# Kernel tuning notes

Measured on AMD Instinct MI355X. Metric: run time of the kernel, lower is better.

## Reference

```python
import jax, jax.numpy as jnp
import numpy as np

M, T, NX, U = 256, 512, 256, 256


def setup_inputs() -> dict:
    key = jax.random.key(0)
    ks = jax.random.split(key, 8)
    u = lambda k, s: jax.random.uniform(k, s, dtype=jnp.float32) * 0.01
    return {
        "x": jax.random.normal(ks[0], (M, T, NX), dtype=jnp.float32),
        "a0": jax.random.normal(ks[1], (M, U), dtype=jnp.float32),
        "wcx": u(ks[2], (NX, U)),
        "wcc": u(ks[3], (U, U)),
        "bc": jnp.zeros((1, U), jnp.float32),
        "wux": u(ks[4], (NX, U)),
        "wuc": u(ks[5], (U, U)),
        "bu": jnp.zeros((1, U), jnp.float32),
        "wrx": u(ks[6], (NX, U)),
        "wrc": u(ks[7], (U, U)),
        "br": jnp.zeros((1, U), jnp.float32),
    }


def reference(x, a0, wcx, wcc, bc, wux, wuc, bu, wrx, wrc, br):
    # x: [m, t, nx] -> scan over time; state c: [m, units]
    def step(c, xt):
        g_u = jax.nn.sigmoid(c @ wuc + xt @ wux + bu)
        g_r = jax.nn.sigmoid(c @ wrc + xt @ wrx + br)
        # NB: original is (g_r * c_prev) @ wcc due to operator precedence
        cand = jnp.tanh((g_r * c) @ wcc + xt @ wcx + bc)
        c_new = g_u * cand + (1.0 - g_u) * c
        return c_new, None

    c_final, _ = jax.lax.scan(step, a0, jnp.swapaxes(x, 0, 1))
    # return_sequences=False, return_state=False -> last hidden state [m, units]
    return c_final
```

## Files before the change

kernel.cpp:

```cpp
#include <hip/hip_runtime.h>

typedef _Float16 h2 __attribute__((ext_vector_type(2)));
typedef _Float16 h4 __attribute__((ext_vector_type(4)));
typedef _Float16 h8 __attribute__((ext_vector_type(8)));
typedef float f4v __attribute__((ext_vector_type(4)));

#define U_DIM 256
#define M_DIM 256
#define T_DIM 512

#if defined(__has_builtin)
#if __has_builtin(__builtin_amdgcn_fdot2)
#define HAVE_FDOT2 1
#endif
#endif

__device__ __forceinline__ float fdot2f(h2 a, h2 b, float c) {
#ifdef HAVE_FDOT2
  return __builtin_amdgcn_fdot2(a, b, c, false);
#else
  return fmaf((float)a[0], (float)b[0], fmaf((float)a[1], (float)b[1], c));
#endif
}

__device__ __forceinline__ float fast_sigmoid(float z) {
  return __builtin_amdgcn_rcpf(1.f + __expf(-z));
}
__device__ __forceinline__ float fast_tanh(float z) {
  return fmaf(2.f, __builtin_amdgcn_rcpf(1.f + __expf(-2.f * z)), -1.f);
}

__global__ void conv_x(const float* __restrict__ x, h8* __restrict__ x16, int n8) {
  int i = blockIdx.x * 256 + threadIdx.x;
  if (i >= n8) return;
  const float4* p = (const float4*)(x + (size_t)i * 8);
  float4 v0 = p[0], v1 = p[1];
  h8 o = {(_Float16)v0.x, (_Float16)v0.y, (_Float16)v0.z, (_Float16)v0.w,
          (_Float16)v1.x, (_Float16)v1.y, (_Float16)v1.z, (_Float16)v1.w};
  x16[i] = o;
}

__global__ void prep_xw(const float* __restrict__ wux, const float* __restrict__ wrx,
                        const float* __restrict__ wcx, h8* __restrict__ wt16) {
  int idx = blockIdx.x * 256 + threadIdx.x;
  int mtx = idx >> 13;
  int rem = idx & 8191;
  int n = rem >> 5;
  int kv = rem & 31;
  const float* W = (mtx == 0) ? wux : ((mtx == 1) ? wrx : wcx);
  h8 o;
#pragma unroll
  for (int e = 0; e < 8; ++e) o[e] = (_Float16)W[(size_t)(kv * 8 + e) * U_DIM + n];
  wt16[idx] = o;
}

__global__ void prep_w(const float* __restrict__ wuc, const float* __restrict__ wrc,
                       const float* __restrict__ wcc, h8* __restrict__ w16) {
  int idx = blockIdx.x * 256 + threadIdx.x;
  int mtx = idx >> 13;
  int rem = idx & 8191;
  int tid = rem >> 4;
  int v   = rem & 15;
  int j = tid >> 1, s = tid & 1;
  const float* W = (mtx == 0) ? wuc : ((mtx == 1) ? wrc : wcc);
  int k0 = 128 * s + 8 * v;
  h8 o;
#pragma unroll
  for (int e = 0; e < 8; ++e) o[e] = (_Float16)W[(size_t)(k0 + e) * U_DIM + j];
  w16[idx] = o;
}

__global__ __launch_bounds__(256, 2)
void xproj_mfma(const h8* __restrict__ x16, const h8* __restrict__ wt16,
                const float* __restrict__ Bu, const float* __restrict__ Br,
                const float* __restrict__ Bc,
                _Float16* __restrict__ XU, _Float16* __restrict__ XR,
                _Float16* __restrict__ XC, int t0, int len) {
  const int mtx = blockIdx.z;
  const float* Bv = (mtx == 0) ? Bu : ((mtx == 1) ? Br : Bc);
  _Float16* O = (mtx == 0) ? XU : ((mtx == 1) ? XR : XC);
  const h8* W = wt16 + (size_t)mtx * 256 * 32;

  __shared__ _Float16 a_sh[128][40];
  __shared__ _Float16 b_sh[128][40];

  const int tid = threadIdx.x;
  const int r0 = blockIdx.x * 128;
  const int c0 = blockIdx.y * 128;

  const int srow = tid >> 1;
  const int spart = tid & 1;
  const int r = r0 + srow;
  const int mm = r / len;
  const int tc = r - mm * len;
  const h8* arow = x16 + ((size_t)mm * T_DIM + (size_t)(t0 + tc)) * 32;
  const h8* brow = W + (size_t)(c0 + srow) * 32;

  const int lane = tid & 63;
  const int w = tid >> 6;
  const int quad = lane >> 4;
  const int mrow = lane & 15;

  f4v acc[2][8];
#pragma unroll
  for (int fr = 0; fr < 2; ++fr)
#pragma unroll
    for (int fc = 0; fc < 8; ++fc) acc[fr][fc] = f4v{0.f, 0.f, 0.f, 0.f};

  for (int k8 = 0; k8 < 32; k8 += 4) {
    h8 a0 = arow[k8 + 2 * spart];
    h8 a1 = arow[k8 + 2 * spart + 1];
    h8 b0 = brow[k8 + 2 * spart];
    h8 b1 = brow[k8 + 2 * spart + 1];
    __syncthreads();
    *(h8*)&a_sh[srow][spart * 16]     = a0;
    *(h8*)&a_sh[srow][spart * 16 + 8] = a1;
    *(h8*)&b_sh[srow][spart * 16]     = b0;
    *(h8*)&b_sh[srow][spart * 16 + 8] = b1;
    __syncthreads();
    h8 af0 = *(const h8*)&a_sh[32 * w + mrow][quad * 8];
    h8 af1 = *(const h8*)&a_sh[32 * w + 16 + mrow][quad * 8];
#pragma unroll
    for (int fc = 0; fc < 8; ++fc) {
      h8 bf = *(const h8*)&b_sh[fc * 16 + mrow][quad * 8];
      acc[0][fc] = __builtin_amdgcn_mfma_f32_16x16x32_f16(af0, bf, acc[0][fc], 0, 0, 0);
      acc[1][fc] = __builtin_amdgcn_mfma_f32_16x16x32_f16(af1, bf, acc[1][fc], 0, 0, 0);
    }
  }

#pragma unroll
  for (int fc = 0; fc < 8; ++fc) {
    int col = c0 + fc * 16 + mrow;
    float bb = Bv[col];
#pragma unroll
    for (int fr = 0; fr < 2; ++fr)
#pragma unroll
      for (int reg = 0; reg < 4; ++reg) {
        int rr = r0 + 32 * w + fr * 16 + quad * 4 + reg;
        O[(size_t)rr * U_DIM + col] = (_Float16)(acc[fr][fc][reg] + bb);
      }
  }
}

__global__ __launch_bounds__(512, 2)
void gru_rec(const _Float16* __restrict__ XU, const _Float16* __restrict__ XR,
             const _Float16* __restrict__ XC, const h8* __restrict__ w16,
             const float* __restrict__ c_in, float* __restrict__ c_out, int len) {
  const int m = blockIdx.x;
  const int tid = threadIdx.x;
  const int j = tid >> 1;
  const int s = tid & 1;
  const int cb = s * 17;
  const int wj = j + ((j >> 7) << 3);

  __shared__ h8 ch8[34];
  __shared__ h8 hh8[34];

  const h8* wub = w16 + (size_t)tid * 16;
  const h8* wrb = wub + 8192;
  const h8* wcb = wub + 16384;

#define DECL_W(i) h8 wu##i = wub[i]; h8 wr##i = wrb[i]; h8 wc##i = wcb[i];
  DECL_W(0)  DECL_W(1)  DECL_W(2)  DECL_W(3)
  DECL_W(4)  DECL_W(5)  DECL_W(6)  DECL_W(7)
  DECL_W(8)  DECL_W(9)  DECL_W(10) DECL_W(11)
  DECL_W(12) DECL_W(13) DECL_W(14) DECL_W(15)
#undef DECL_W

  float cj = c_in[m * U_DIM + j];
  if (s == 0) ((_Float16*)ch8)[wj] = (_Float16)cj;

  const _Float16* XUb = XU + (size_t)m * len * U_DIM;
  const _Float16* XRb = XR + (size_t)m * len * U_DIM;
  const _Float16* XCb = XC + (size_t)m * len * U_DIM;

  int off = j;
  float xuv = (float)XUb[off], xrv = (float)XRb[off], xcv = (float)XCb[off];

  __syncthreads();

  for (int t = 0; t < len; ++t) {
    int offn = off + ((t + 1 < len) ? U_DIM : 0);
    float nxu = (float)XUb[offn], nxr = (float)XRb[offn], nxc = (float)XCb[offn];

    float pu0 = 0.f, pu1 = 0.f, pr0 = 0.f, pr1 = 0.f;
#define PASS1(i) { h8 cv = ch8[cb + i];                                   \
    pu0 = fdot2f(h2{cv[0], cv[1]}, h2{wu##i[0], wu##i[1]}, pu0);          \
    pr0 = fdot2f(h2{cv[0], cv[1]}, h2{wr##i[0], wr##i[1]}, pr0);          \
    pu1 = fdot2f(h2{cv[2], cv[3]}, h2{wu##i[2], wu##i[3]}, pu1);          \
    pr1 = fdot2f(h2{cv[2], cv[3]}, h2{wr##i[2], wr##i[3]}, pr1);          \
    pu0 = fdot2f(h2{cv[4], cv[5]}, h2{wu##i[4], wu##i[5]}, pu0);          \
    pr0 = fdot2f(h2{cv[4], cv[5]}, h2{wr##i[4], wr##i[5]}, pr0);          \
    pu1 = fdot2f(h2{cv[6], cv[7]}, h2{wu##i[6], wu##i[7]}, pu1);          \
    pr1 = fdot2f(h2{cv[6], cv[7]}, h2{wr##i[6], wr##i[7]}, pr1); }
    PASS1(0)  PASS1(1)  PASS1(2)  PASS1(3)
    PASS1(4)  PASS1(5)  PASS1(6)  PASS1(7)
    PASS1(8)  PASS1(9)  PASS1(10) PASS1(11)
    PASS1(12) PASS1(13) PASS1(14) PASS1(15)
#undef PASS1

    float pu = pu0 + pu1;
    pu += __shfl_xor(pu, 1);
    float pr = pr0 + pr1;
    pr += __shfl_xor(pr, 1);

    float gu = fast_sigmoid(pu + xuv);
    float gr = fast_sigmoid(pr + xrv);
    if (s == 0) ((_Float16*)hh8)[wj] = (_Float16)(gr * cj);
    __syncthreads();

    float pc0 = 0.f, pc1 = 0.f;
#define PASS2(i) { h8 hv = hh8[cb + i];                                   \
    pc0 = fdot2f(h2{hv[0], hv[1]}, h2{wc##i[0], wc##i[1]}, pc0);          \
    pc1 = fdot2f(h2{hv[2], hv[3]}, h2{wc##i[2], wc##i[3]}, pc1);          \
    pc0 = fdot2f(h2{hv[4], hv[5]}, h2{wc##i[4], wc##i[5]}, pc0);          \
    pc1 = fdot2f(h2{hv[6], hv[7]}, h2{wc##i[6], wc##i[7]}, pc1); }
    PASS2(0)  PASS2(1)  PASS2(2)  PASS2(3)
    PASS2(4)  PASS2(5)  PASS2(6)  PASS2(7)
    PASS2(8)  PASS2(9)  PASS2(10) PASS2(11)
    PASS2(12) PASS2(13) PASS2(14) PASS2(15)
#undef PASS2

    float pc = pc0 + pc1;
    pc += __shfl_xor(pc, 1);

    float cand = fast_tanh(pc + xcv);
    cj = fmaf(gu, cand - cj, cj);
    if (s == 0) ((_Float16*)ch8)[wj] = (_Float16)cj;

    xuv = nxu; xrv = nxr; xcv = nxc; off = offn;
    __syncthreads();
  }

  if (s == 0) c_out[m * U_DIM + j] = cj;
}

extern "C" void kernel_launch(void* const* d_in, const int* in_sizes, int n_in,
                              void* d_out, int out_size, void* d_ws, size_t ws_size,
                              hipStream_t stream) {
  const float* x   = (const float*)d_in[0];
  const float* a0  = (const float*)d_in[1];
  const float* wcx = (const float*)d_in[2];
  const float* wcc = (const float*)d_in[3];
  const float* bc  = (const float*)d_in[4];
  const float* wux = (const float*)d_in[5];
  const float* wuc = (const float*)d_in[6];
  const float* bu  = (const float*)d_in[7];
  const float* wrx = (const float*)d_in[8];
  const float* wrc = (const float*)d_in[9];
  const float* br  = (const float*)d_in[10];
  float* out = (float*)d_out;

  const size_t x16_bytes = (size_t)M_DIM * T_DIM * U_DIM * 2;
  const size_t wt_bytes  = 3ull * 256 * 32 * 16;
  const size_t w16_bytes = 3ull * 512 * 16 * 16;
  const size_t fixed = x16_bytes + wt_bytes + w16_bytes;

  h8* x16  = (h8*)d_ws;
  h8* wt16 = (h8*)((char*)d_ws + x16_bytes);
  h8* w16  = (h8*)((char*)d_ws + x16_bytes + wt_bytes);
  _Float16* XU0 = (_Float16*)((char*)d_ws + fixed);

  size_t avail = (ws_size > fixed) ? (ws_size - fixed) : 0;
  const size_t perT = 3ull * M_DIM * U_DIM * 2;
  int Tc = (int)(avail / perT);
  if (Tc > T_DIM) Tc = T_DIM;
  if (Tc < 1) Tc = 1;
  int nch = (T_DIM + Tc - 1) / Tc;
  Tc = (T_DIM + nch - 1) / nch;

  _Float16* XU = XU0;
  _Float16* XR = XU + (size_t)M_DIM * Tc * U_DIM;
  _Float16* XC = XR + (size_t)M_DIM * Tc * U_DIM;

  conv_x<<<16384, 256, 0, stream>>>(x, x16, M_DIM * T_DIM * U_DIM / 8);
  prep_xw<<<96, 256, 0, stream>>>(wux, wrx, wcx, wt16);
  prep_w<<<96, 256, 0, stream>>>(wuc, wrc, wcc, w16);

  for (int t0 = 0; t0 < T_DIM; t0 += Tc) {
    int lenc = (T_DIM - t0) < Tc ? (T_DIM - t0) : Tc;
    dim3 g((M_DIM * lenc) / 128, 2, 3);
    xproj_mfma<<<g, 256, 0, stream>>>(x16, wt16, bu, br, bc,
                                      XU, XR, XC, t0, lenc);
    gru_rec<<<M_DIM, 512, 0, stream>>>(XU, XR, XC, w16,
                                       (t0 == 0 ? a0 : out), out, lenc);
  }
}
```

Measured before the change: 967.8 us.

## Split GRU recurrent matvec over 8-lane groups computing 4 outputs each with DPP reductions

```diff
diff --git a/kernel.cpp b/kernel.cpp
--- a/kernel.cpp
+++ b/kernel.cpp
@@ -28,6 +28,18 @@
 }
 __device__ __forceinline__ float fast_tanh(float z) {
   return fmaf(2.f, __builtin_amdgcn_rcpf(1.f + __expf(-2.f * z)), -1.f);
+}
+
+template <int CTRL>
+__device__ __forceinline__ float dpp_xadd(float x) {
+  int y = __builtin_amdgcn_update_dpp(0, __float_as_int(x), CTRL, 0xF, 0xF, true);
+  return x + __int_as_float(y);
+}
+__device__ __forceinline__ float reduce8(float x) {
+  x = dpp_xadd<0xB1>(x);
+  x = dpp_xadd<0x4E>(x);
+  x = dpp_xadd<0x141>(x);
+  return x;
 }
 
 __global__ void conv_x(const float* __restrict__ x, h8* __restrict__ x16, int n8) {
@@ -60,14 +72,16 @@
   int mtx = idx >> 13;
   int rem = idx & 8191;
   int tid = rem >> 4;
-  int v   = rem & 15;
-  int j = tid >> 1, s = tid & 1;
+  int q   = rem & 15;
+  int o = q >> 2, v = q & 3;
+  int g = tid >> 3, s = tid & 7;
   const float* W = (mtx == 0) ? wuc : ((mtx == 1) ? wrc : wcc);
-  int k0 = 128 * s + 8 * v;
-  h8 o;
-#pragma unroll
-  for (int e = 0; e < 8; ++e) o[e] = (_Float16)W[(size_t)(k0 + e) * U_DIM + j];
-  w16[idx] = o;
+  int col = 4 * g + o;
+  int k0 = 32 * s + 8 * v;
+  h8 out;
+#pragma unroll
+  for (int e = 0; e < 8; ++e) out[e] = (_Float16)W[(size_t)(k0 + e) * U_DIM + col];
+  w16[idx] = out;
 }
 
 __global__ __launch_bounds__(256, 2)
@@ -148,19 +162,24 @@
              const float* __restrict__ c_in, float* __restrict__ c_out, int len) {
   const int m = blockIdx.x;
   const int tid = threadIdx.x;
-  const int j = tid >> 1;
-  const int s = tid & 1;
-  const int cb = s * 17;
-  const int wj = j + ((j >> 7) << 3);
-
-  __shared__ h8 ch8[34];
-  __shared__ h8 hh8[34];
+  const int g = tid >> 3;
+  const int s = tid & 7;
+  const int so = s & 3;
+  const int cb = 5 * s;
+  const int j = 4 * g + so;
+  const int hwj = 40 * (j >> 5) + (j & 31);
+  const bool wr_lane = (s < 4);
+
+  __shared__ h8 ch8[40];
+  __shared__ h8 hh8[40];
+  _Float16* cwp = (_Float16*)ch8;
+  _Float16* hwp = (_Float16*)hh8;
 
   const h8* wub = w16 + (size_t)tid * 16;
   const h8* wrb = wub + 8192;
   const h8* wcb = wub + 16384;
 
-#define DECL_W(i) h8 wu##i = wub[i]; h8 wr##i = wrb[i]; h8 wc##i = wcb[i];
+#define DECL_W(l) h8 wu##l = wub[l]; h8 wr##l = wrb[l]; h8 wc##l = wcb[l];
   DECL_W(0)  DECL_W(1)  DECL_W(2)  DECL_W(3)
   DECL_W(4)  DECL_W(5)  DECL_W(6)  DECL_W(7)
   DECL_W(8)  DECL_W(9)  DECL_W(10) DECL_W(11)
@@ -168,7 +187,7 @@
 #undef DECL_W
 
   float cj = c_in[m * U_DIM + j];
-  if (s == 0) ((_Float16*)ch8)[wj] = (_Float16)cj;
+  if (wr_lane) cwp[hwj] = (_Float16)cj;
 
   const _Float16* XUb = XU + (size_t)m * len * U_DIM;
   const _Float16* XRb = XR + (size_t)m * len * U_DIM;
@@ -179,60 +198,70 @@
 
   __syncthreads();
 
+#define P1O(cv, l, o)                                                     \
+  pu##o = fdot2f(h2{cv[0], cv[1]}, h2{wu##l[0], wu##l[1]}, pu##o);        \
+  pu##o = fdot2f(h2{cv[2], cv[3]}, h2{wu##l[2], wu##l[3]}, pu##o);        \
+  pu##o = fdot2f(h2{cv[4], cv[5]}, h2{wu##l[4], wu##l[5]}, pu##o);        \
+  pu##o = fdot2f(h2{cv[6], cv[7]}, h2{wu##l[6], wu##l[7]}, pu##o);        \
+  pr##o = fdot2f(h2{cv[0], cv[1]}, h2{wr##l[0], wr##l[1]}, pr##o);        \
+  pr##o = fdot2f(h2{cv[2], cv[3]}, h2{wr##l[2], wr##l[3]}, pr##o);        \
+  pr##o = fdot2f(h2{cv[4], cv[5]}, h2{wr##l[4], wr##l[5]}, pr##o);        \
+  pr##o = fdot2f(h2{cv[6], cv[7]}, h2{wr##l[6], wr##l[7]}, pr##o);
+#define PASS1V(v, la, lb, lc, ld) { h8 cv = ch8[cb + v];                  \
+  P1O(cv, la, 0) P1O(cv, lb, 1) P1O(cv, lc, 2) P1O(cv, ld, 3) }
+
+#define P2O(hv, l, o)                                                     \
+  pc##o = fdot2f(h2{hv[0], hv[1]}, h2{wc##l[0], wc##l[1]}, pc##o);        \
+  pc##o = fdot2f(h2{hv[2], hv[3]}, h2{wc##l[2], wc##l[3]}, pc##o);        \
+  pc##o = fdot2f(h2{hv[4], hv[5]}, h2{wc##l[4], wc##l[5]}, pc##o);        \
+  pc##o = fdot2f(h2{hv[6], hv[7]}, h2{wc##l[6], wc##l[7]}, pc##o);
+#define PASS2V(v, la, lb, lc, ld) { h8 hv = hh8[cb + v];                  \
+  P2O(hv, la, 0) P2O(hv, lb, 1) P2O(hv, lc, 2) P2O(hv, ld, 3) }
+
   for (int t = 0; t < len; ++t) {
     int offn = off + ((t + 1 < len) ? U_DIM : 0);
     float nxu = (float)XUb[offn], nxr = (float)XRb[offn], nxc = (float)XCb[offn];
 
-    float pu0 = 0.f, pu1 = 0.f, pr0 = 0.f, pr1 = 0.f;
-#define PASS1(i) { h8 cv = ch8[cb + i];                                   \
-    pu0 = fdot2f(h2{cv[0], cv[1]}, h2{wu##i[0], wu##i[1]}, pu0);          \
-    pr0 = fdot2f(h2{cv[0], cv[1]}, h2{wr##i[0], wr##i[1]}, pr0);          \
-    pu1 = fdot2f(h2{cv[2], cv[3]}, h2{wu##i[2], wu##i[3]}, pu1);          \
-    pr1 = fdot2f(h2{cv[2], cv[3]}, h2{wr##i[2], wr##i[3]}, pr1);          \
-    pu0 = fdot2f(h2{cv[4], cv[5]}, h2{wu##i[4], wu##i[5]}, pu0);          \
-    pr0 = fdot2f(h2{cv[4], cv[5]}, h2{wr##i[4], wr##i[5]}, pr0);          \
-    pu1 = fdot2f(h2{cv[6], cv[7]}, h2{wu##i[6], wu##i[7]}, pu1);          \
-    pr1 = fdot2f(h2{cv[6], cv[7]}, h2{wr##i[6], wr##i[7]}, pr1); }
-    PASS1(0)  PASS1(1)  PASS1(2)  PASS1(3)
-    PASS1(4)  PASS1(5)  PASS1(6)  PASS1(7)
-    PASS1(8)  PASS1(9)  PASS1(10) PASS1(11)
-    PASS1(12) PASS1(13) PASS1(14) PASS1(15)
-#undef PASS1
-
-    float pu = pu0 + pu1;
-    pu += __shfl_xor(pu, 1);
-    float pr = pr0 + pr1;
-    pr += __shfl_xor(pr, 1);
-
-    float gu = fast_sigmoid(pu + xuv);
-    float gr = fast_sigmoid(pr + xrv);
-    if (s == 0) ((_Float16*)hh8)[wj] = (_Float16)(gr * cj);
+    float pu0 = 0.f, pu1 = 0.f, pu2 = 0.f, pu3 = 0.f;
+    float pr0 = 0.f, pr1 = 0.f, pr2 = 0.f, pr3 = 0.f;
+    PASS1V(0, 0, 4, 8, 12)
+    PASS1V(1, 1, 5, 9, 13)
+    PASS1V(2, 2, 6, 10, 14)
+    PASS1V(3, 3, 7, 11, 15)
+
+    pu0 = reduce8(pu0); pu1 = reduce8(pu1); pu2 = reduce8(pu2); pu3 = reduce8(pu3);
+    pr0 = reduce8(pr0); pr1 = reduce8(pr1); pr2 = reduce8(pr2); pr3 = reduce8(pr3);
+
+    float puj = (so & 2) ? ((so & 1) ? pu3 : pu2) : ((so & 1) ? pu1 : pu0);
+    float prj = (so & 2) ? ((so & 1) ? pr3 : pr2) : ((so & 1) ? pr1 : pr0);
+    float gu = fast_sigmoid(puj + xuv);
+    float gr = fast_sigmoid(prj + xrv);
+    if (wr_lane) hwp[hwj] = (_Float16)(gr * cj);
     __syncthreads();
 
-    float pc0 = 0.f, pc1 = 0.f;
-#define PASS2(i) { h8 hv = hh8[cb + i];                                   \
-    pc0 = fdot2f(h2{hv[0], hv[1]}, h2{wc##i[0], wc##i[1]}, pc0);          \
-    pc1 = fdot2f(h2{hv[2], hv[3]}, h2{wc##i[2], wc##i[3]}, pc1);          \
-    pc0 = fdot2f(h2{hv[4], hv[5]}, h2{wc##i[4], wc##i[5]}, pc0);          \
-    pc1 = fdot2f(h2{hv[6], hv[7]}, h2{wc##i[6], wc##i[7]}, pc1); }
-    PASS2(0)  PASS2(1)  PASS2(2)  PASS2(3)
-    PASS2(4)  PASS2(5)  PASS2(6)  PASS2(7)
-    PASS2(8)  PASS2(9)  PASS2(10) PASS2(11)
-    PASS2(12) PASS2(13) PASS2(14) PASS2(15)
-#undef PASS2
-
-    float pc = pc0 + pc1;
-    pc += __shfl_xor(pc, 1);
-
-    float cand = fast_tanh(pc + xcv);
+    float pc0 = 0.f, pc1 = 0.f, pc2 = 0.f, pc3 = 0.f;
+    PASS2V(0, 0, 4, 8, 12)
+    PASS2V(1, 1, 5, 9, 13)
+    PASS2V(2, 2, 6, 10, 14)
+    PASS2V(3, 3, 7, 11, 15)
+
+    pc0 = reduce8(pc0); pc1 = reduce8(pc1); pc2 = reduce8(pc2); pc3 = reduce8(pc3);
+    float pcj = (so & 2) ? ((so & 1) ? pc3 : pc2) : ((so & 1) ? pc1 : pc0);
+
+    float cand = fast_tanh(pcj + xcv);
     cj = fmaf(gu, cand - cj, cj);
-    if (s == 0) ((_Float16*)ch8)[wj] = (_Float16)cj;
+    if (wr_lane) cwp[hwj] = (_Float16)cj;
 
     xuv = nxu; xrv = nxr; xcv = nxc; off = offn;
     __syncthreads();
   }
 
-  if (s == 0) c_out[m * U_DIM + j] = cj;
+#undef P1O
+#undef PASS1V
+#undef P2O
+#undef PASS2V
+
+  if (wr_lane) c_out[m * U_DIM + j] = cj;
 }
 
 extern "C" void kernel_launch(void* const* d_in, const int* in_sizes, int n_in,
```

After: 957.1 us. No clear change (-1.1%).

## Batch 16 sequences per block and use MFMA for recurrent matmuls

Applied to the files above, without the earlier changes.

```diff
diff --git a/kernel.cpp b/kernel.cpp
--- a/kernel.cpp
+++ b/kernel.cpp
@@ -1,27 +1,11 @@
 #include <hip/hip_runtime.h>
 
-typedef _Float16 h2 __attribute__((ext_vector_type(2)));
-typedef _Float16 h4 __attribute__((ext_vector_type(4)));
 typedef _Float16 h8 __attribute__((ext_vector_type(8)));
 typedef float f4v __attribute__((ext_vector_type(4)));
 
 #define U_DIM 256
 #define M_DIM 256
 #define T_DIM 512
-
-#if defined(__has_builtin)
-#if __has_builtin(__builtin_amdgcn_fdot2)
-#define HAVE_FDOT2 1
-#endif
-#endif
-
-__device__ __forceinline__ float fdot2f(h2 a, h2 b, float c) {
-#ifdef HAVE_FDOT2
-  return __builtin_amdgcn_fdot2(a, b, c, false);
-#else
-  return fmaf((float)a[0], (float)b[0], fmaf((float)a[1], (float)b[1], c));
-#endif
-}
 
 __device__ __forceinline__ float fast_sigmoid(float z) {
   return __builtin_amdgcn_rcpf(1.f + __expf(-z));
@@ -59,14 +43,15 @@
   int idx = blockIdx.x * 256 + threadIdx.x;
   int mtx = idx >> 13;
   int rem = idx & 8191;
-  int tid = rem >> 4;
-  int v   = rem & 15;
-  int j = tid >> 1, s = tid & 1;
+  int nt = rem >> 9;
+  int kblk = (rem >> 6) & 7;
+  int ln = rem & 63;
   const float* W = (mtx == 0) ? wuc : ((mtx == 1) ? wrc : wcc);
-  int k0 = 128 * s + 8 * v;
+  int col = nt * 16 + (ln & 15);
+  int k0 = kblk * 32 + ((ln >> 4) << 3);
   h8 o;
 #pragma unroll
-  for (int e = 0; e < 8; ++e) o[e] = (_Float16)W[(size_t)(k0 + e) * U_DIM + j];
+  for (int e = 0; e < 8; ++e) o[e] = (_Float16)W[(size_t)(k0 + e) * U_DIM + col];
   w16[idx] = o;
 }
 
@@ -146,93 +131,122 @@
 void gru_rec(const _Float16* __restrict__ XU, const _Float16* __restrict__ XR,
              const _Float16* __restrict__ XC, const h8* __restrict__ w16,
              const float* __restrict__ c_in, float* __restrict__ c_out, int len) {
-  const int m = blockIdx.x;
   const int tid = threadIdx.x;
-  const int j = tid >> 1;
-  const int s = tid & 1;
-  const int cb = s * 17;
-  const int wj = j + ((j >> 7) << 3);
-
-  __shared__ h8 ch8[34];
-  __shared__ h8 hh8[34];
-
-  const h8* wub = w16 + (size_t)tid * 16;
+  const int lane = tid & 63;
+  const int wv = tid >> 6;
+  const int M0 = blockIdx.x * 16;
+  const int rowq = lane >> 4;
+  const int nlo = lane & 15;
+  const int n0 = 32 * wv;
+
+  __shared__ _Float16 c_sh[16][264];
+  __shared__ _Float16 h_sh[16][264];
+  __shared__ h8 wc_sh[8192];
+
+  const h8* wcg = w16 + 16384;
+#pragma unroll
+  for (int it = 0; it < 16; ++it) wc_sh[512 * it + tid] = wcg[512 * it + tid];
+
+  const h8* wub = w16 + (size_t)wv * 1024 + lane;
   const h8* wrb = wub + 8192;
-  const h8* wcb = wub + 16384;
-
-#define DECL_W(i) h8 wu##i = wub[i]; h8 wr##i = wrb[i]; h8 wc##i = wcb[i];
-  DECL_W(0)  DECL_W(1)  DECL_W(2)  DECL_W(3)
-  DECL_W(4)  DECL_W(5)  DECL_W(6)  DECL_W(7)
-  DECL_W(8)  DECL_W(9)  DECL_W(10) DECL_W(11)
-  DECL_W(12) DECL_W(13) DECL_W(14) DECL_W(15)
-#undef DECL_W
-
-  float cj = c_in[m * U_DIM + j];
-  if (s == 0) ((_Float16*)ch8)[wj] = (_Float16)cj;
-
-  const _Float16* XUb = XU + (size_t)m * len * U_DIM;
-  const _Float16* XRb = XR + (size_t)m * len * U_DIM;
-  const _Float16* XCb = XC + (size_t)m * len * U_DIM;
-
-  int off = j;
-  float xuv = (float)XUb[off], xrv = (float)XRb[off], xcv = (float)XCb[off];
+  h8 wu[2][8], wr[2][8];
+#pragma unroll
+  for (int i = 0; i < 2; ++i)
+#pragma unroll
+    for (int k = 0; k < 8; ++k) {
+      wu[i][k] = wub[(i * 8 + k) * 64];
+      wr[i][k] = wrb[(i * 8 + k) * 64];
+    }
+
+  float creg[2][4];
+  unsigned goff[2][4];
+#pragma unroll
+  for (int i = 0; i < 2; ++i)
+#pragma unroll
+    for (int q = 0; q < 4; ++q) {
+      int mr = rowq * 4 + q;
+      int col = n0 + 16 * i + nlo;
+      float cv = c_in[(M0 + mr) * U_DIM + col];
+      creg[i][q] = cv;
+      c_sh[mr][col] = (_Float16)cv;
+      goff[i][q] = ((unsigned)((M0 + mr) * len) * U_DIM + (unsigned)col) * 2u;
+    }
+
+  const char* xu_c = (const char*)XU;
+  const char* xr_c = (const char*)XR;
+  const char* xc_c = (const char*)XC;
+
+  const _Float16* cAb = &c_sh[0][0] + (nlo * 264 + rowq * 8);
+  const _Float16* hAb = &h_sh[0][0] + (nlo * 264 + rowq * 8);
+  const h8* wcb = &wc_sh[0] + (size_t)wv * 1024 + lane;
 
   __syncthreads();
 
   for (int t = 0; t < len; ++t) {
-    int offn = off + ((t + 1 < len) ? U_DIM : 0);
-    float nxu = (float)XUb[offn], nxr = (float)XRb[offn], nxc = (float)XCb[offn];
-
-    float pu0 = 0.f, pu1 = 0.f, pr0 = 0.f, pr1 = 0.f;
-#define PASS1(i) { h8 cv = ch8[cb + i];                                   \
-    pu0 = fdot2f(h2{cv[0], cv[1]}, h2{wu##i[0], wu##i[1]}, pu0);          \
-    pr0 = fdot2f(h2{cv[0], cv[1]}, h2{wr##i[0], wr##i[1]}, pr0);          \
-    pu1 = fdot2f(h2{cv[2], cv[3]}, h2{wu##i[2], wu##i[3]}, pu1);          \
-    pr1 = fdot2f(h2{cv[2], cv[3]}, h2{wr##i[2], wr##i[3]}, pr1);          \
-    pu0 = fdot2f(h2{cv[4], cv[5]}, h2{wu##i[4], wu##i[5]}, pu0);          \
-    pr0 = fdot2f(h2{cv[4], cv[5]}, h2{wr##i[4], wr##i[5]}, pr0);          \
-    pu1 = fdot2f(h2{cv[6], cv[7]}, h2{wu##i[6], wu##i[7]}, pu1);          \
-    pr1 = fdot2f(h2{cv[6], cv[7]}, h2{wr##i[6], wr##i[7]}, pr1); }
-    PASS1(0)  PASS1(1)  PASS1(2)  PASS1(3)
-    PASS1(4)  PASS1(5)  PASS1(6)  PASS1(7)
-    PASS1(8)  PASS1(9)  PASS1(10) PASS1(11)
-    PASS1(12) PASS1(13) PASS1(14) PASS1(15)
-#undef PASS1
-
-    float pu = pu0 + pu1;
-    pu += __shfl_xor(pu, 1);
-    float pr = pr0 + pr1;
-    pr += __shfl_xor(pr, 1);
-
-    float gu = fast_sigmoid(pu + xuv);
-    float gr = fast_sigmoid(pr + xrv);
-    if (s == 0) ((_Float16*)hh8)[wj] = (_Float16)(gr * cj);
+    float xu[2][4], xr[2][4], xc[2][4];
+#pragma unroll
+    for (int i = 0; i < 2; ++i)
+#pragma unroll
+      for (int q = 0; q < 4; ++q) {
+        unsigned o = goff[i][q];
+        xu[i][q] = (float)*(const _Float16*)(xu_c + o);
+        xr[i][q] = (float)*(const _Float16*)(xr_c + o);
+        xc[i][q] = (float)*(const _Float16*)(xc_c + o);
+      }
+
+    f4v aU[2], aR[2];
+#pragma unroll
+    for (int i = 0; i < 2; ++i) { aU[i] = f4v{0.f,0.f,0.f,0.f}; aR[i] = f4v{0.f,0.f,0.f,0.f}; }
+#pragma unroll
+    for (int k = 0; k < 8; ++k) {
+      h8 A = *(const h8*)(cAb + k * 32);
+      aU[0] = __builtin_amdgcn_mfma_f32_16x16x32_f16(A, wu[0][k], aU[0], 0, 0, 0);
+      aU[1] = __builtin_amdgcn_mfma_f32_16x16x32_f16(A, wu[1][k], aU[1], 0, 0, 0);
+      aR[0] = __builtin_amdgcn_mfma_f32_16x16x32_f16(A, wr[0][k], aR[0], 0, 0, 0);
+      aR[1] = __builtin_amdgcn_mfma_f32_16x16x32_f16(A, wr[1][k], aR[1], 0, 0, 0);
+    }
+
+    float gu[2][4];
+#pragma unroll
+    for (int i = 0; i < 2; ++i)
+#pragma unroll
+      for (int q = 0; q < 4; ++q) {
+        float gu_ = fast_sigmoid(aU[i][q] + xu[i][q]);
+        float gr_ = fast_sigmoid(aR[i][q] + xr[i][q]);
+        gu[i][q] = gu_;
+        h_sh[rowq * 4 + q][n0 + 16 * i + nlo] = (_Float16)(gr_ * creg[i][q]);
+      }
     __syncthreads();
 
-    float pc0 = 0.f, pc1 = 0.f;
-#define PASS2(i) { h8 hv = hh8[cb + i];                                   \
-    pc0 = fdot2f(h2{hv[0], hv[1]}, h2{wc##i[0], wc##i[1]}, pc0);          \
-    pc1 = fdot2f(h2{hv[2], hv[3]}, h2{wc##i[2], wc##i[3]}, pc1);          \
-    pc0 = fdot2f(h2{hv[4], hv[5]}, h2{wc##i[4], wc##i[5]}, pc0);          \
-    pc1 = fdot2f(h2{hv[6], hv[7]}, h2{wc##i[6], wc##i[7]}, pc1); }
-    PASS2(0)  PASS2(1)  PASS2(2)  PASS2(3)
-    PASS2(4)  PASS2(5)  PASS2(6)  PASS2(7)
-    PASS2(8)  PASS2(9)  PASS2(10) PASS2(11)
-    PASS2(12) PASS2(13) PASS2(14) PASS2(15)
-#undef PASS2
-
-    float pc = pc0 + pc1;
-    pc += __shfl_xor(pc, 1);
-
-    float cand = fast_tanh(pc + xcv);
-    cj = fmaf(gu, cand - cj, cj);
-    if (s == 0) ((_Float16*)ch8)[wj] = (_Float16)cj;
-
-    xuv = nxu; xrv = nxr; xcv = nxc; off = offn;
+    f4v aC[2];
+#pragma unroll
+    for (int i = 0; i < 2; ++i) aC[i] = f4v{0.f,0.f,0.f,0.f};
+#pragma unroll
+    for (int k = 0; k < 8; ++k) {
+      h8 A = *(const h8*)(hAb + k * 32);
+      aC[0] = __builtin_amdgcn_mfma_f32_16x16x32_f16(A, wcb[k * 64], aC[0], 0, 0, 0);
+      aC[1] = __builtin_amdgcn_mfma_f32_16x16x32_f16(A, wcb[512 + k * 64], aC[1], 0, 0, 0);
+    }
+
+#pragma unroll
+    for (int i = 0; i < 2; ++i)
+#pragma unroll
+      for (int q = 0; q < 4; ++q) {
+        float cd = fast_tanh(aC[i][q] + xc[i][q]);
+        float cn = fmaf(gu[i][q], cd - creg[i][q], creg[i][q]);
+        creg[i][q] = cn;
+        c_sh[rowq * 4 + q][n0 + 16 * i + nlo] = (_Float16)cn;
+      }
+
+    xu_c += U_DIM * 2; xr_c += U_DIM * 2; xc_c += U_DIM * 2;
     __syncthreads();
   }
 
-  if (s == 0) c_out[m * U_DIM + j] = cj;
+#pragma unroll
+  for (int i = 0; i < 2; ++i)
+#pragma unroll
+    for (int q = 0; q < 4; ++q)
+      c_out[(M0 + rowq * 4 + q) * U_DIM + (n0 + 16 * i + nlo)] = creg[i][q];
 }
 
 extern "C" void kernel_launch(void* const* d_in, const int* in_sizes, int n_in,
@@ -253,7 +267,7 @@
 
   const size_t x16_bytes = (size_t)M_DIM * T_DIM * U_DIM * 2;
   const size_t wt_bytes  = 3ull * 256 * 32 * 16;
-  const size_t w16_bytes = 3ull * 512 * 16 * 16;
+  const size_t w16_bytes = 3ull * 16 * 8 * 64 * 16;
   const size_t fixed = x16_bytes + wt_bytes + w16_bytes;
 
   h8* x16  = (h8*)d_ws;
@@ -282,7 +296,7 @@
     dim3 g((M_DIM * lenc) / 128, 2, 3);
     xproj_mfma<<<g, 256, 0, stream>>>(x16, wt16, bu, br, bc,
                                       XU, XR, XC, t0, lenc);
-    gru_rec<<<M_DIM, 512, 0, stream>>>(XU, XR, XC, w16,
-                                       (t0 == 0 ? a0 : out), out, lenc);
+    gru_rec<<<16, 512, 0, stream>>>(XU, XR, XC, w16,
+                                    (t0 == 0 ? a0 : out), out, lenc);
   }
 }
```

Result: slower. 3.478 ms (+259.4%).
